# Optimization experiments

Hardware: AMD Instinct MI355X
Metric: run time of the kernel (lower is better)

## Reference

```python
import math
import jax, jax.numpy as jnp
import numpy as np

B, S, D, H = 2, 2048, 2048, 16
HD = D // H
INV_NORM = 1.0 / math.sqrt(HD)


def _build_alibi(batch, n_heads, seq_len):
    # Standard BLOOM ALiBi slopes (n_heads is a power of two here)
    base = 2.0 ** (-(2.0 ** -(math.log2(n_heads) - 3)))
    slopes = base ** np.arange(1, n_heads + 1, dtype=np.float32)  # [H]
    pos = np.arange(seq_len, dtype=np.float32)  # [S]
    alibi = slopes[:, None] * pos[None, :]  # [H, S]
    alibi = np.broadcast_to(alibi[None], (batch, n_heads, seq_len)).reshape(batch * n_heads, 1, seq_len)
    return jnp.asarray(alibi)


def _build_causal_mask(batch, seq_len):
    neg = jnp.float32(-1e9)
    tril = jnp.tril(jnp.ones((seq_len, seq_len), dtype=bool))
    mask = jnp.where(tril, jnp.float32(0.0), neg)  # [S, S]
    return jnp.broadcast_to(mask[None, None], (batch, 1, seq_len, seq_len))


def setup_inputs() -> dict:
    key = jax.random.key(0)
    ks = jax.random.split(key, 6)
    scale = 0.02
    return {
        "hidden_states": jax.random.normal(ks[0], (B, S, D), jnp.float32),
        "residual": jax.random.normal(ks[1], (B, S, D), jnp.float32),
        "alibi": _build_alibi(B, H, S),
        "attention_mask": _build_causal_mask(B, S),
        "W_qkv": jax.random.normal(ks[2], (3 * D, D), jnp.float32) * scale,
        "b_qkv": jax.random.normal(ks[3], (3 * D,), jnp.float32) * scale,
        "W_dense": jax.random.normal(ks[4], (D, D), jnp.float32) * scale,
        "b_dense": jax.random.normal(ks[5], (D,), jnp.float32) * scale,
    }


def reference(hidden_states, residual, alibi, attention_mask, W_qkv, b_qkv, W_dense, b_dense):
    b, s, d = hidden_states.shape
    # fused QKV projection: [B,S,3D] -> [B,S,H,3,HD]
    fused = (hidden_states @ W_qkv.T + b_qkv).reshape(b, s, H, 3, HD)
    q = fused[..., 0, :].transpose(0, 2, 1, 3)  # [B,H,S,HD]
    k = fused[..., 1, :].transpose(0, 2, 1, 3)
    v = fused[..., 2, :].transpose(0, 2, 1, 3)
    # baddbmm: alibi + inv_norm * q @ k^T ; alibi is [B*H,1,S] -> broadcast over q_len
    scores = alibi.reshape(b, H, 1, s) + INV_NORM * jnp.einsum("bhqd,bhkd->bhqk", q, k)
    scores = scores + attention_mask  # additive causal mask [B,1,S,S]
    probs = jax.nn.softmax(scores.astype(jnp.float32), axis=-1).astype(hidden_states.dtype)
    ctx = jnp.einsum("bhqk,bhkd->bhqd", probs, v)  # [B,H,S,HD]
    ctx = ctx.transpose(0, 2, 1, 3).reshape(b, s, d)  # merge heads
    out = ctx @ W_dense.T + b_dense
    return out + residual  # dropout_add with p=0 (eval)
```

## Files before the change

kernel.cpp:

```cpp
#include <hip/hip_runtime.h>
#include <hip/hip_bf16.h>

typedef __hip_bfloat16 bf16;
typedef __attribute__((ext_vector_type(8))) short s8v;
typedef __attribute__((ext_vector_type(4))) float f4v;

#define B_  2
#define S_  2048
#define D_  2048
#define H_  16
#define HD_ 128
#define INV_NORM 0.08838834764831845f

static __device__ __forceinline__ f4v mfma16(s8v a, s8v b, f4v c) {
    return __builtin_amdgcn_mfma_f32_16x16x32_bf16(a, b, c, 0, 0, 0);
}

static __device__ __forceinline__ void gload_lds(const void* gp, void* lp) {
    __builtin_amdgcn_global_load_lds(
        (const __attribute__((address_space(1))) unsigned int*)gp,
        (__attribute__((address_space(3))) unsigned int*)lp, 16, 0, 0);
}

__global__ __launch_bounds__(256)
void cvt_f32_bf16(const float* __restrict__ src, bf16* __restrict__ dst, int n4)
{
    int i = blockIdx.x * 256 + threadIdx.x;
    if (i < n4) {
        float4 f = ((const float4*)src)[i];
        union { ushort4 u4; bf16 h[4]; } p;
        p.h[0] = __float2bfloat16(f.x);
        p.h[1] = __float2bfloat16(f.y);
        p.h[2] = __float2bfloat16(f.z);
        p.h[3] = __float2bfloat16(f.w);
        ((ushort4*)dst)[i] = p.u4;
    }
}

#define VMW(s) asm volatile("s_waitcnt " s ::: "memory")
#define BARR() { __builtin_amdgcn_s_barrier(); asm volatile("" ::: "memory"); }

#define RD_A(dst, mibase)                                                       \
  _Pragma("unroll") for (int mi = 0; mi < 4; ++mi) {                            \
    dst[mi][0] = *(const s8v*)(lds + bufB + aR + (mibase + mi) * 4096 + sx0);   \
    dst[mi][1] = *(const s8v*)(lds + bufB + aR + (mibase + mi) * 4096 + sx1);   \
  }
#define RD_B(njbase)                                                            \
  _Pragma("unroll") for (int nj = 0; nj < 2; ++nj) {                            \
    bfr[nj][0] = *(const s8v*)(lds + bufB + bRo + (njbase + nj) * 8192 + sx0);  \
    bfr[nj][1] = *(const s8v*)(lds + bufB + bRo + (njbase + nj) * 8192 + sx1);  \
  }
#define MM(af, mibase, njbase)                                                  \
  __builtin_amdgcn_s_setprio(1);                                                \
  _Pragma("unroll") for (int mi = 0; mi < 4; ++mi)                              \
  _Pragma("unroll") for (int nj = 0; nj < 2; ++nj) {                            \
    acc[mibase + mi][njbase + nj] =                                             \
        mfma16(af[mi][0], bfr[nj][0], acc[mibase + mi][njbase + nj]);           \
    acc[mibase + mi][njbase + nj] =                                             \
        mfma16(af[mi][1], bfr[nj][1], acc[mibase + mi][njbase + nj]);           \
  }                                                                             \
  __builtin_amdgcn_s_setprio(0);

#define KTILE(DOPRE, VA, VB, VC)                                                \
  {                                                                             \
    const int bufB = cur << 16, bufN = (cur ^ 1) << 16;                         \
    const size_t t1 = (size_t)(kt + 1) * 64;                                    \
                          \
    if (DOPRE) { gload_lds(gA + t1 + srcO0, lds + bufN + 0 + dst0);             \
                 gload_lds(gA + t1 + srcO1, lds + bufN + 0 + dst1); }           \
    VMW(VA); BARR();                                                            \
    RD_A(a0, 0); RD_B(0);                                                       \
    MM(a0, 0, 0);                                                               \
                               \
    if (DOPRE) { gload_lds(gB + t1 + srcO0, lds + bufN + 32768 + dst0);         \
                 gload_lds(gB + t1 + srcO1, lds + bufN + 32768 + dst1); }       \
    VMW(VB); BARR();                                                            \
    RD_A(a1, 4);                                                                \
    MM(a1, 4, 0);                                                               \
                               \
    if (DOPRE) { gload_lds(gA2 + t1 + srcO0, lds + bufN + 16384 + dst0);        \
                 gload_lds(gA2 + t1 + srcO1, lds + bufN + 16384 + dst1); }      \
    VMW(VC); BARR();                                                            \
    RD_B(2);                                                                    \
    MM(a0, 0, 2);                                                               \
    BARR();     \
                         \
    if (DOPRE) { gload_lds(gB2 + t1 + srcO0, lds + bufN + 49152 + dst0);        \
                 gload_lds(gB2 + t1 + srcO1, lds + bufN + 49152 + dst1); }      \
    MM(a1, 4, 2);                                                               \
  }

__global__ __launch_bounds__(512, 2)
void gemm_qkv8(const bf16* __restrict__ A, const bf16* __restrict__ Bw,
               const float* __restrict__ bias,
               bf16* __restrict__ o0, bf16* __restrict__ o1, bf16* __restrict__ o2)
{
    __shared__ __align__(16) char lds[131072];
    const int tid  = threadIdx.x;
    const int wave = tid >> 6, lane = tid & 63;
    const int col  = lane & 15, quad = lane >> 4;
    const int wr   = wave >> 2, wc = wave & 3;

    int id = (int)blockIdx.y * 24 + (int)blockIdx.x;
    id = (id & 7) * 48 + (id >> 3);
    const int bm = id / 24, bn = id % 24;

    const bf16* gA  = A  + (size_t)bm * 256 * 2048;
    const bf16* gA2 = gA + (size_t)128 * 2048;
    const bf16* gB  = Bw + (size_t)bn * 256 * 2048;
    const bf16* gB2 = gB + (size_t)128 * 2048;

    const int r0   = tid >> 3, bk0 = tid & 7;
    const int srcO0 = r0 * 2048 + ((bk0 ^ (r0 & 7)) << 3);
    const int srcO1 = srcO0 + 64 * 2048;
    const int dst0 = tid * 16, dst1 = dst0 + 8192;

    const int sx0 = ((quad ^ (col & 7)) << 4);
    const int sx1 = (((4 + quad) ^ (col & 7)) << 4);
    const int aR  = (wr * 16 + col) * 128;
    const int bRo = (wc * 16 + col) * 128 + 32768;

    const f4v fzero = {0.f, 0.f, 0.f, 0.f};
    f4v acc[8][4];
#pragma unroll
    for (int i = 0; i < 8; i++)
#pragma unroll
        for (int j = 0; j < 4; j++) acc[i][j] = fzero;
    s8v a0[4][2], a1[4][2], bfr[2][2];

    gload_lds(gA  + srcO0, lds + 0     + dst0);
    gload_lds(gA  + srcO1, lds + 0     + dst1);
    gload_lds(gB  + srcO0, lds + 32768 + dst0);
    gload_lds(gB  + srcO1, lds + 32768 + dst1);
    gload_lds(gA2 + srcO0, lds + 16384 + dst0);
    gload_lds(gA2 + srcO1, lds + 16384 + dst1);
    gload_lds(gB2 + srcO0, lds + 49152 + dst0);
    gload_lds(gB2 + srcO1, lds + 49152 + dst1);

    int cur = 0;
    for (int kt = 0; kt < 31; ++kt) {
        KTILE(1, "vmcnt(6)", "vmcnt(6)", "vmcnt(6)");
        cur ^= 1;
    }
    {
        const int kt = 31;
        KTILE(0, "vmcnt(4)", "vmcnt(2)", "vmcnt(0)");
    }

#pragma unroll
    for (int mi = 0; mi < 8; ++mi) {
#pragma unroll
        for (int nj = 0; nj < 4; ++nj) {
            const int cg = bn * 2 + (nj >> 1);
            const int t3 = cg % 3, hh = cg / 3;
            const int hd = (nj & 1) * 64 + wc * 16 + col;
            const float bv = bias[cg * 128 + hd];
            const int r = bm * 256 + mi * 32 + wr * 16 + (quad << 2);
            const int bi = r >> 11, srow = r & (S_ - 1);
            if (t3 == 2) {
                union { ushort4 u4; bf16 hv[4]; } pk;
#pragma unroll
                for (int rg = 0; rg < 4; ++rg)
                    pk.hv[rg] = __float2bfloat16(acc[mi][nj][rg] + bv);
                *(ushort4*)(o2 + ((size_t)(bi * H_ + hh) * HD_ + hd) * S_ + srow) = pk.u4;
            } else {
                bf16* dst = (t3 == 0) ? o0 : o1;
#pragma unroll
                for (int rg = 0; rg < 4; ++rg)
                    dst[((size_t)(bi * H_ + hh) * S_ + (srow + rg)) * HD_ + hd] =
                        __float2bfloat16(acc[mi][nj][rg] + bv);
            }
        }
    }
}

#define STAGE_D(gptr, t, choff)                                                 \
  { const size_t co = (size_t)(t) * 64;                                         \
    gload_lds(gptr + co + srcO0, lds + ((t) & 1) * 49152 + (choff) + dst0);     \
    gload_lds(gptr + co + srcO1, lds + ((t) & 1) * 49152 + (choff) + dst1); }

#define DKTILE(P1, P2, VA)                                                      \
  {                                                                             \
    const int bufB = (kt & 1) * 49152;                                          \
    VMW(VA); BARR();                                                            \
    if (P1) STAGE_D(gA2, kt + 1, 16384);                                        \
    _Pragma("unroll") for (int mi = 0; mi < 2; ++mi) {                          \
      alo[mi][0] = *(const s8v*)(lds + bufB + aR + mi * 8192 + sx0);            \
      alo[mi][1] = *(const s8v*)(lds + bufB + aR + mi * 8192 + sx1);            \
    }                                                                           \
    _Pragma("unroll") for (int nj = 0; nj < 4; ++nj) {                          \
      bfr[nj][0] = *(const s8v*)(lds + bufB + bR + nj * 4096 + sx0);            \
      bfr[nj][1] = *(const s8v*)(lds + bufB + bR + nj * 4096 + sx1);            \
    }                                                                           \
    __builtin_amdgcn_s_setprio(1);                                              \
    _Pragma("unroll") for (int mi = 0; mi < 2; ++mi)                            \
    _Pragma("unroll") for (int nj = 0; nj < 4; ++nj) {                          \
      acc[mi][nj] = mfma16(alo[mi][0], bfr[nj][0], acc[mi][nj]);                \
      acc[mi][nj] = mfma16(alo[mi][1], bfr[nj][1], acc[mi][nj]);                \
    }                                                                           \
    __builtin_amdgcn_s_setprio(0);                                              \
    BARR();                                                                     \
    if (P2) { STAGE_D(gA, kt + 2, 0); STAGE_D(gB, kt + 2, 32768); }             \
    _Pragma("unroll") for (int mi = 0; mi < 2; ++mi) {                          \
      ahi[mi][0] = *(const s8v*)(lds + bufB + 16384 + aR + mi * 8192 + sx0);    \
      ahi[mi][1] = *(const s8v*)(lds + bufB + 16384 + aR + mi * 8192 + sx1);    \
    }                                                                           \
    __builtin_amdgcn_s_setprio(1);                                              \
    _Pragma("unroll") for (int mi = 0; mi < 2; ++mi)                            \
    _Pragma("unroll") for (int nj = 0; nj < 4; ++nj) {                          \
      acc[2 + mi][nj] = mfma16(ahi[mi][0], bfr[nj][0], acc[2 + mi][nj]);        \
      acc[2 + mi][nj] = mfma16(ahi[mi][1], bfr[nj][1], acc[2 + mi][nj]);        \
    }                                                                           \
    __builtin_amdgcn_s_setprio(0);                                              \
  }

__global__ __launch_bounds__(512, 2)
void gemm_dense8(const bf16* __restrict__ A, const bf16* __restrict__ Bw,
                 const float* __restrict__ bias, const float* __restrict__ resid,
                 float* __restrict__ of)
{
    __shared__ __align__(16) char lds[98304];
    const int tid  = threadIdx.x;
    const int wave = tid >> 6, lane = tid & 63;
    const int col  = lane & 15, quad = lane >> 4;
    const int wr   = wave >> 1, wc = wave & 1;

    int id = (int)blockIdx.y * 16 + (int)blockIdx.x;
    id = (id & 7) * 32 + (id >> 3);
    const int bm = id >> 4, bn = id & 15;

    const bf16* gA  = A  + (size_t)bm * 256 * 2048;
    const bf16* gA2 = gA + (size_t)128 * 2048;
    const bf16* gB  = Bw + (size_t)bn * 128 * 2048;

    const int r0   = tid >> 3, bk0 = tid & 7;
    const int srcO0 = r0 * 2048 + ((bk0 ^ (r0 & 7)) << 3);
    const int srcO1 = srcO0 + 64 * 2048;
    const int dst0 = tid * 16, dst1 = dst0 + 8192;

    const int sx0 = ((quad ^ (col & 7)) << 4);
    const int sx1 = (((4 + quad) ^ (col & 7)) << 4);
    const int aR  = (wr * 16 + col) * 128;
    const int bR  = (wc * 16 + col) * 128 + 32768;

    const f4v fzero = {0.f, 0.f, 0.f, 0.f};
    f4v acc[4][4];
#pragma unroll
    for (int i = 0; i < 4; i++)
#pragma unroll
        for (int j = 0; j < 4; j++) acc[i][j] = fzero;
    s8v alo[2][2], ahi[2][2], bfr[4][2];

    STAGE_D(gA,  0, 0);
    STAGE_D(gB,  0, 32768);
    STAGE_D(gA2, 0, 16384);
    STAGE_D(gA,  1, 0);
    STAGE_D(gB,  1, 32768);

    for (int kt = 0; kt < 30; ++kt) {
        DKTILE(1, 1, "vmcnt(4)");
    }
    {   const int kt = 30;
        DKTILE(1, 0, "vmcnt(4)");
    }
    {   const int kt = 31;
        DKTILE(0, 0, "vmcnt(0)");
    }

#pragma unroll
    for (int mi = 0; mi < 4; ++mi) {
#pragma unroll
        for (int nj = 0; nj < 4; ++nj) {
            const int c = bn * 128 + nj * 32 + wc * 16 + col;
            const float bv = bias[c];
            const int r = bm * 256 + mi * 64 + wr * 16 + (quad << 2);
#pragma unroll
            for (int rg = 0; rg < 4; ++rg) {
                const size_t idx = (size_t)(r + rg) * D_ + c;
                of[idx] = acc[mi][nj][rg] + bv + resid[idx];
            }
        }
    }
}

__global__ __launch_bounds__(256, 2)
void attn(const bf16* __restrict__ Qb, const bf16* __restrict__ Kb,
          const bf16* __restrict__ Vt, bf16* __restrict__ ctx)
{
    __shared__ __align__(16) char Ksm[2][64 * 256];
    __shared__ __align__(16) char Vsm[2][128 * 128];
    __shared__ __align__(16) char Pl[4 * 16 * 128];

    const int x = blockIdx.x;
    const int bh = blockIdx.y;
    const int u = (bh >> 3) & 1;
    const int qb = u ? x : (int)gridDim.x - 1 - x;
    const int b = bh >> 4, h = bh & 15;
    const int tid = threadIdx.x;
    const int wave = tid >> 6, lane = tid & 63;
    const int col = lane & 15, quad = lane >> 4;
    const int q0 = qb << 6;
    const int qg = q0 + wave * 16 + col;
    const float slope = exp2f(-0.5f * (float)(h + 1));
    const int sw = (col & 7) << 4;

    const bf16* Qp = Qb + ((size_t)bh * S_ + q0 + wave * 16) * HD_;
    s8v aq[4];
#pragma unroll
    for (int c = 0; c < 4; c++)
        aq[c] = *(const s8v*)(Qp + (size_t)col * HD_ + c * 32 + quad * 8);

    const f4v fzero = {0.f, 0.f, 0.f, 0.f};
    f4v o[8];
#pragma unroll
    for (int t = 0; t < 8; t++) o[t] = fzero;
    float m = -1e30f, l = 0.f;

    const bf16* Kbase = Kb + (size_t)bh * S_ * HD_;
    const bf16* Vbase = Vt + (size_t)bh * HD_ * S_;

    int ksrc[4], vsrc[4];
#pragma unroll
    for (int p = 0; p < 4; p++) {
        const int g = p * 256 + tid;
        const int kr = g >> 4, kb = g & 15;
        ksrc[p] = kr * HD_ + ((kb ^ (kr & 7)) << 3);
        const int vr = g >> 3, vb = g & 7;
        vsrc[p] = vr * S_ + ((vb ^ (vr & 7)) << 3);
    }
    const int ldst = tid << 4;

    {
        const bf16* Kp = Kbase;
        const bf16* Vp = Vbase;
#pragma unroll
        for (int p = 0; p < 4; p++) {
            gload_lds(Kp + ksrc[p], Ksm[0] + p * 4096 + ldst);
            gload_lds(Vp + vsrc[p], Vsm[0] + p * 4096 + ldst);
        }
    }
    __syncthreads();

    const int nkt = qb + 1;
    for (int kt = 0; kt < nkt; kt++) {
        const int cur = kt & 1;
        const int k0 = kt << 6;

        if (kt + 1 < nkt) {
            const bf16* Kp = Kbase + (size_t)(kt + 1) * 64 * HD_;
            const bf16* Vp = Vbase + (kt + 1) * 64;
            char* Kd = Ksm[cur ^ 1];
            char* Vd = Vsm[cur ^ 1];
#pragma unroll
            for (int p = 0; p < 4; p++) {
                gload_lds(Kp + ksrc[p], Kd + p * 4096 + ldst);
                gload_lds(Vp + vsrc[p], Vd + p * 4096 + ldst);
            }
        }
        const char* Kcur = Ksm[cur];
        const char* Vcur = Vsm[cur];

        f4v sc[4];
        __builtin_amdgcn_s_setprio(1);
#pragma unroll
        for (int st = 0; st < 4; st++) {
            sc[st] = fzero;
#pragma unroll
            for (int c = 0; c < 4; c++) {
                const s8v kf = *(const s8v*)(Kcur + (st * 16 + col) * 256 +
                                             ((c * 64 + quad * 16) ^ sw));
                sc[st] = mfma16(kf, aq[c], sc[st]);
            }
        }
        __builtin_amdgcn_s_setprio(0);

        float s[16];
        float mx = -1e30f;
#pragma unroll
        for (int st = 0; st < 4; st++)
#pragma unroll
            for (int r = 0; r < 4; r++) {
                const int key = k0 + st * 16 + (quad << 2) + r;
                float v = sc[st][r] * INV_NORM + slope * (float)key;
                v = (key > qg) ? -1e9f : v;
                s[st * 4 + r] = v;
                mx = fmaxf(mx, v);
            }
        mx = fmaxf(mx, __shfl_xor(mx, 16));
        mx = fmaxf(mx, __shfl_xor(mx, 32));
        const float nm = fmaxf(m, mx);
        float ps = 0.f;
#pragma unroll
        for (int i = 0; i < 16; i++) { s[i] = __expf(s[i] - nm); ps += s[i]; }
        ps += __shfl_xor(ps, 16);
        ps += __shfl_xor(ps, 32);
        const float alpha = __expf(m - nm);
        l = l * alpha + ps;
        m = nm;
#pragma unroll
        for (int t = 0; t < 8; t++) o[t] *= alpha;

        char* plw = Pl + wave * 2048 + col * 128;
#pragma unroll
        for (int st = 0; st < 4; st++) {
            union { ushort4 u4; bf16 hh[4]; } pk;
#pragma unroll
            for (int r = 0; r < 4; r++) pk.hh[r] = __float2bfloat16(s[st * 4 + r]);
            *(ushort4*)(plw + ((st * 32 + quad * 8) ^ sw)) = pk.u4;
        }
        const s8v pf0 = *(const s8v*)(plw + ((quad * 16) ^ sw));
        const s8v pf1 = *(const s8v*)(plw + ((64 + quad * 16) ^ sw));

        __builtin_amdgcn_s_setprio(1);
#pragma unroll
        for (int t = 0; t < 8; t++) {
            const s8v vf0 = *(const s8v*)(Vcur + (t * 16 + col) * 128 +
                                          ((quad * 16) ^ sw));
            o[t] = mfma16(vf0, pf0, o[t]);
            const s8v vf1 = *(const s8v*)(Vcur + (t * 16 + col) * 128 +
                                          ((64 + quad * 16) ^ sw));
            o[t] = mfma16(vf1, pf1, o[t]);
        }
        __builtin_amdgcn_s_setprio(0);

        __syncthreads();
    }

    const float rl = 1.0f / l;
#pragma unroll
    for (int t = 0; t < 8; t++) {
        union { ushort4 u4; bf16 hh[4]; } pk;
#pragma unroll
        for (int r = 0; r < 4; r++) pk.hh[r] = __float2bfloat16(o[t][r] * rl);
        *(ushort4*)&ctx[((size_t)(b * S_) + qg) * D_ + h * HD_ + t * 16 + (quad << 2)] =
            pk.u4;
    }
}

extern "C" void kernel_launch(void* const* d_in, const int* in_sizes, int n_in,
                              void* d_out, int out_size, void* d_ws, size_t ws_size,
                              hipStream_t stream)
{
    const float* hs    = (const float*)d_in[0];
    const float* resid = (const float*)d_in[1];
    const float* Wqkv  = (const float*)d_in[4];
    const float* bqkv  = (const float*)d_in[5];
    const float* Wd    = (const float*)d_in[6];
    const float* bd    = (const float*)d_in[7];
    float* out = (float*)d_out;

    const size_t seg  = (size_t)B_ * H_ * S_ * HD_;
    const size_t nHS  = (size_t)B_ * S_ * D_;
    const size_t nWq  = (size_t)3 * D_ * D_;
    const size_t nWd  = (size_t)D_ * D_;
    bf16* Qbuf = (bf16*)d_ws;
    bf16* Kbuf = Qbuf + seg;
    bf16* Vtb  = Kbuf + seg;
    bf16* ctx  = Vtb + seg;
    bf16* hsb  = ctx + seg;
    bf16* Wqb  = hsb + nHS;
    bf16* Wdb  = Wqb + nWq;

    cvt_f32_bf16<<<(int)(nHS / 4 + 255) / 256, 256, 0, stream>>>(hs, hsb, (int)(nHS / 4));
    cvt_f32_bf16<<<(int)(nWq / 4 + 255) / 256, 256, 0, stream>>>(Wqkv, Wqb, (int)(nWq / 4));
    cvt_f32_bf16<<<(int)(nWd / 4 + 255) / 256, 256, 0, stream>>>(Wd, Wdb, (int)(nWd / 4));

    gemm_qkv8<<<dim3(24, 16), 512, 0, stream>>>(hsb, Wqb, bqkv, Qbuf, Kbuf, Vtb);
    attn<<<dim3(32, 32), 256, 0, stream>>>(Qbuf, Kbuf, Vtb, ctx);
    gemm_dense8<<<dim3(16, 16), 512, 0, stream>>>(ctx, Wdb, bd, resid, out);
}
```

Measured before the change: 425.0 us.

## Retile QKV GEMM to 256x192 blocks with a deeper, split-staged LDS pipeline

The QKV projection GEMM now uses 256x192 output tiles (grid 32x16 = 512 blocks) instead of 256x256 (384 blocks). This gives a more even wave count across the 256 CUs and cuts LDS to 112 KB. The K loop is restructured to prefetch two tiles ahead: the A2 half for kt+1 is issued mid-tile and A/B for kt+2 after the first barrier, with two barriers per k-tile instead of four. The epilogue recomputes the column-to-head mapping for the 48-column-per-wave layout. The risk is lower arithmetic intensity per block and a trickier vmcnt accounting.

```diff
diff --git a/kernel.cpp b/kernel.cpp
--- a/kernel.cpp
+++ b/kernel.cpp
@@ -40,121 +40,114 @@
 #define VMW(s) asm volatile("s_waitcnt " s ::: "memory")
 #define BARR() { __builtin_amdgcn_s_barrier(); asm volatile("" ::: "memory"); }
 
-#define RD_A(dst, mibase)                                                       \
-  _Pragma("unroll") for (int mi = 0; mi < 4; ++mi) {                            \
-    dst[mi][0] = *(const s8v*)(lds + bufB + aR + (mibase + mi) * 4096 + sx0);   \
-    dst[mi][1] = *(const s8v*)(lds + bufB + aR + (mibase + mi) * 4096 + sx1);   \
+#define QSTAGE2(gptr, t, choff)                                                 \
+  { const size_t co = (size_t)(t) * 64;                                         \
+    gload_lds(gptr + co + srcO0, lds + ((t) & 1) * 57344 + (choff) + dst0);     \
+    gload_lds(gptr + co + srcO1, lds + ((t) & 1) * 57344 + (choff) + dst1); }
+#define QSTAGE3(gptr, t, choff)                                                 \
+  { const size_t co = (size_t)(t) * 64;                                         \
+    gload_lds(gptr + co + srcO0, lds + ((t) & 1) * 57344 + (choff) + dst0);     \
+    gload_lds(gptr + co + srcO1, lds + ((t) & 1) * 57344 + (choff) + dst1);     \
+    gload_lds(gptr + co + srcO2, lds + ((t) & 1) * 57344 + (choff) + dst2); }
+
+#define QKTILE(P1, P2, VA)                                                      \
+  {                                                                             \
+    const int bufB = (kt & 1) * 57344;                                          \
+    VMW(VA); BARR();                                                            \
+    if (P1) QSTAGE2(gA2, kt + 1, 16384);                                        \
+    _Pragma("unroll") for (int mi = 0; mi < 4; ++mi) {                          \
+      a0[mi][0] = *(const s8v*)(lds + bufB + aR + mi * 4096 + sx0);             \
+      a0[mi][1] = *(const s8v*)(lds + bufB + aR + mi * 4096 + sx1);             \
+    }                                                                           \
+    _Pragma("unroll") for (int nj = 0; nj < 3; ++nj) {                          \
+      bfr[nj][0] = *(const s8v*)(lds + bufB + bR + nj * 2048 + sx0);            \
+      bfr[nj][1] = *(const s8v*)(lds + bufB + bR + nj * 2048 + sx1);            \
+    }                                                                           \
+    __builtin_amdgcn_s_setprio(1);                                              \
+    _Pragma("unroll") for (int mi = 0; mi < 4; ++mi)                            \
+    _Pragma("unroll") for (int nj = 0; nj < 3; ++nj) {                          \
+      acc[mi][nj] = mfma16(a0[mi][0], bfr[nj][0], acc[mi][nj]);                 \
+      acc[mi][nj] = mfma16(a0[mi][1], bfr[nj][1], acc[mi][nj]);                 \
+    }                                                                           \
+    __builtin_amdgcn_s_setprio(0);                                              \
+    BARR();                                                                     \
+    if (P2) { QSTAGE2(gA, kt + 2, 0); QSTAGE3(gB, kt + 2, 32768); }             \
+    _Pragma("unroll") for (int mi = 0; mi < 4; ++mi) {                          \
+      a1[mi][0] = *(const s8v*)(lds + bufB + aR + (4 + mi) * 4096 + sx0);       \
+      a1[mi][1] = *(const s8v*)(lds + bufB + aR + (4 + mi) * 4096 + sx1);       \
+    }                                                                           \
+    __builtin_amdgcn_s_setprio(1);                                              \
+    _Pragma("unroll") for (int mi = 0; mi < 4; ++mi)                            \
+    _Pragma("unroll") for (int nj = 0; nj < 3; ++nj) {                          \
+      acc[4 + mi][nj] = mfma16(a1[mi][0], bfr[nj][0], acc[4 + mi][nj]);         \
+      acc[4 + mi][nj] = mfma16(a1[mi][1], bfr[nj][1], acc[4 + mi][nj]);         \
+    }                                                                           \
+    __builtin_amdgcn_s_setprio(0);                                              \
   }
-#define RD_B(njbase)                                                            \
-  _Pragma("unroll") for (int nj = 0; nj < 2; ++nj) {                            \
-    bfr[nj][0] = *(const s8v*)(lds + bufB + bRo + (njbase + nj) * 8192 + sx0);  \
-    bfr[nj][1] = *(const s8v*)(lds + bufB + bRo + (njbase + nj) * 8192 + sx1);  \
-  }
-#define MM(af, mibase, njbase)                                                  \
-  __builtin_amdgcn_s_setprio(1);                                                \
-  _Pragma("unroll") for (int mi = 0; mi < 4; ++mi)                              \
-  _Pragma("unroll") for (int nj = 0; nj < 2; ++nj) {                            \
-    acc[mibase + mi][njbase + nj] =                                             \
-        mfma16(af[mi][0], bfr[nj][0], acc[mibase + mi][njbase + nj]);           \
-    acc[mibase + mi][njbase + nj] =                                             \
-        mfma16(af[mi][1], bfr[nj][1], acc[mibase + mi][njbase + nj]);           \
-  }                                                                             \
-  __builtin_amdgcn_s_setprio(0);
-
-#define KTILE(DOPRE, VA, VB, VC)                                                \
-  {                                                                             \
-    const int bufB = cur << 16, bufN = (cur ^ 1) << 16;                         \
-    const size_t t1 = (size_t)(kt + 1) * 64;                                    \
-                          \
-    if (DOPRE) { gload_lds(gA + t1 + srcO0, lds + bufN + 0 + dst0);             \
-                 gload_lds(gA + t1 + srcO1, lds + bufN + 0 + dst1); }           \
-    VMW(VA); BARR();                                                            \
-    RD_A(a0, 0); RD_B(0);                                                       \
-    MM(a0, 0, 0);                                                               \
-                               \
-    if (DOPRE) { gload_lds(gB + t1 + srcO0, lds + bufN + 32768 + dst0);         \
-                 gload_lds(gB + t1 + srcO1, lds + bufN + 32768 + dst1); }       \
-    VMW(VB); BARR();                                                            \
-    RD_A(a1, 4);                                                                \
-    MM(a1, 4, 0);                                                               \
-                               \
-    if (DOPRE) { gload_lds(gA2 + t1 + srcO0, lds + bufN + 16384 + dst0);        \
-                 gload_lds(gA2 + t1 + srcO1, lds + bufN + 16384 + dst1); }      \
-    VMW(VC); BARR();                                                            \
-    RD_B(2);                                                                    \
-    MM(a0, 0, 2);                                                               \
-    BARR();     \
-                         \
-    if (DOPRE) { gload_lds(gB2 + t1 + srcO0, lds + bufN + 49152 + dst0);        \
-                 gload_lds(gB2 + t1 + srcO1, lds + bufN + 49152 + dst1); }      \
-    MM(a1, 4, 2);                                                               \
-  }
 
 __global__ __launch_bounds__(512, 2)
-void gemm_qkv8(const bf16* __restrict__ A, const bf16* __restrict__ Bw,
+void gemm_qkv9(const bf16* __restrict__ A, const bf16* __restrict__ Bw,
                const float* __restrict__ bias,
                bf16* __restrict__ o0, bf16* __restrict__ o1, bf16* __restrict__ o2)
 {
-    __shared__ __align__(16) char lds[131072];
+    __shared__ __align__(16) char lds[114688];
     const int tid  = threadIdx.x;
     const int wave = tid >> 6, lane = tid & 63;
     const int col  = lane & 15, quad = lane >> 4;
     const int wr   = wave >> 2, wc = wave & 3;
 
-    int id = (int)blockIdx.y * 24 + (int)blockIdx.x;
-    id = (id & 7) * 48 + (id >> 3);
-    const int bm = id / 24, bn = id % 24;
+    int id = (int)blockIdx.y * 32 + (int)blockIdx.x;
+    id = (id & 7) * 64 + (id >> 3);
+    const int bm = id >> 5, bn = id & 31;
 
     const bf16* gA  = A  + (size_t)bm * 256 * 2048;
     const bf16* gA2 = gA + (size_t)128 * 2048;
-    const bf16* gB  = Bw + (size_t)bn * 256 * 2048;
-    const bf16* gB2 = gB + (size_t)128 * 2048;
+    const bf16* gB  = Bw + (size_t)bn * 192 * 2048;
 
     const int r0   = tid >> 3, bk0 = tid & 7;
     const int srcO0 = r0 * 2048 + ((bk0 ^ (r0 & 7)) << 3);
     const int srcO1 = srcO0 + 64 * 2048;
-    const int dst0 = tid * 16, dst1 = dst0 + 8192;
+    const int srcO2 = srcO0 + 128 * 2048;
+    const int dst0 = tid * 16, dst1 = dst0 + 8192, dst2 = dst0 + 16384;
 
     const int sx0 = ((quad ^ (col & 7)) << 4);
     const int sx1 = (((4 + quad) ^ (col & 7)) << 4);
     const int aR  = (wr * 16 + col) * 128;
-    const int bRo = (wc * 16 + col) * 128 + 32768;
+    const int bR  = (wc * 48 + col) * 128 + 32768;
 
     const f4v fzero = {0.f, 0.f, 0.f, 0.f};
-    f4v acc[8][4];
+    f4v acc[8][3];
 #pragma unroll
     for (int i = 0; i < 8; i++)
 #pragma unroll
-        for (int j = 0; j < 4; j++) acc[i][j] = fzero;
-    s8v a0[4][2], a1[4][2], bfr[2][2];
-
-    gload_lds(gA  + srcO0, lds + 0     + dst0);
-    gload_lds(gA  + srcO1, lds + 0     + dst1);
-    gload_lds(gB  + srcO0, lds + 32768 + dst0);
-    gload_lds(gB  + srcO1, lds + 32768 + dst1);
-    gload_lds(gA2 + srcO0, lds + 16384 + dst0);
-    gload_lds(gA2 + srcO1, lds + 16384 + dst1);
-    gload_lds(gB2 + srcO0, lds + 49152 + dst0);
-    gload_lds(gB2 + srcO1, lds + 49152 + dst1);
-
-    int cur = 0;
-    for (int kt = 0; kt < 31; ++kt) {
-        KTILE(1, "vmcnt(6)", "vmcnt(6)", "vmcnt(6)");
-        cur ^= 1;
-    }
-    {
-        const int kt = 31;
-        KTILE(0, "vmcnt(4)", "vmcnt(2)", "vmcnt(0)");
+        for (int j = 0; j < 3; j++) acc[i][j] = fzero;
+    s8v a0[4][2], a1[4][2], bfr[3][2];
+
+    QSTAGE2(gA,  0, 0);
+    QSTAGE3(gB,  0, 32768);
+    QSTAGE2(gA2, 0, 16384);
+    QSTAGE2(gA,  1, 0);
+    QSTAGE3(gB,  1, 32768);
+
+    for (int kt = 0; kt < 30; ++kt) {
+        QKTILE(1, 1, "vmcnt(5)");
+    }
+    {   const int kt = 30;
+        QKTILE(1, 0, "vmcnt(5)");
+    }
+    {   const int kt = 31;
+        QKTILE(0, 0, "vmcnt(0)");
     }
 
 #pragma unroll
     for (int mi = 0; mi < 8; ++mi) {
 #pragma unroll
-        for (int nj = 0; nj < 4; ++nj) {
-            const int cg = bn * 2 + (nj >> 1);
+        for (int nj = 0; nj < 3; ++nj) {
+            const int c  = bn * 192 + wc * 48 + nj * 16 + col;
+            const int cg = c >> 7;
             const int t3 = cg % 3, hh = cg / 3;
-            const int hd = (nj & 1) * 64 + wc * 16 + col;
-            const float bv = bias[cg * 128 + hd];
+            const int hd = c & 127;
+            const float bv = bias[c];
             const int r = bm * 256 + mi * 32 + wr * 16 + (quad << 2);
             const int bi = r >> 11, srow = r & (S_ - 1);
             if (t3 == 2) {
@@ -465,7 +458,7 @@
     cvt_f32_bf16<<<(int)(nWq / 4 + 255) / 256, 256, 0, stream>>>(Wqkv, Wqb, (int)(nWq / 4));
     cvt_f32_bf16<<<(int)(nWd / 4 + 255) / 256, 256, 0, stream>>>(Wd, Wdb, (int)(nWd / 4));
 
-    gemm_qkv8<<<dim3(24, 16), 512, 0, stream>>>(hsb, Wqb, bqkv, Qbuf, Kbuf, Vtb);
+    gemm_qkv9<<<dim3(32, 16), 512, 0, stream>>>(hsb, Wqb, bqkv, Qbuf, Kbuf, Vtb);
     attn<<<dim3(32, 32), 256, 0, stream>>>(Qbuf, Kbuf, Vtb, ctx);
     gemm_dense8<<<dim3(16, 16), 512, 0, stream>>>(ctx, Wdb, bd, resid, out);
 }
```

New measurement: 428.4 us. Within noise of the previous version (+0.8%).
